# Kernel optimization log

Measured on AMD Instinct MI355X. Metric: run time of the kernel, lower is better.

The kernel has to match this reference:

```python
import jax, jax.numpy as jnp
import numpy as np

N = 50000      # nodes
D = 64         # hidden
EMB = 16       # emb_dims
E = 800000     # edges = N * knn(16)
R2 = 0.3 ** 2  # r^2 at epoch 0
GW = 1.0       # grav_weight at epoch 0
EPS = 1e-5


def _lin_params(k, fi, fo):
    kw, kb = jax.random.split(k)
    W = jax.random.normal(kw, (fi, fo), jnp.float32) / np.sqrt(fi).astype(np.float32)
    b = jax.random.normal(kb, (fo,), jnp.float32) * 0.01
    return W, b


def setup_inputs() -> dict:
    key = jax.random.key(0)
    ks = jax.random.split(key, 16)
    inp = {}
    inp['hidden_features'] = jax.random.normal(ks[0], (N, D), jnp.float32)
    inp['edge_index'] = jax.random.randint(ks[1], (2, E), 0, N, jnp.int32)
    inp['current_epoch'] = 0
    # spatial network: (D+1)->D->D->EMB, each Linear + LayerNorm + ReLU
    for i, (fi, fo) in enumerate([(D + 1, D), (D, D), (D, EMB)]):
        W, b = _lin_params(ks[2 + i], fi, fo)
        inp[f'sW{i}'] = W
        inp[f'sb{i}'] = b
        inp[f'sg{i}'] = jnp.ones((fo,), jnp.float32)
        inp[f'sB{i}'] = jnp.zeros((fo,), jnp.float32)
    # feature network: 2*(D+1)->D->D, each Linear + LayerNorm + ReLU
    for i, (fi, fo) in enumerate([(2 * (D + 1), D), (D, D)]):
        W, b = _lin_params(ks[8 + i], fi, fo)
        inp[f'fW{i}'] = W
        inp[f'fb{i}'] = b
        inp[f'fg{i}'] = jnp.ones((fo,), jnp.float32)
        inp[f'fB{i}'] = jnp.zeros((fo,), jnp.float32)
    return inp


def _ln(x, g, b):
    m = jnp.mean(x, axis=-1, keepdims=True)
    v = jnp.mean((x - m) ** 2, axis=-1, keepdims=True)
    return (x - m) * jax.lax.rsqrt(v + EPS) * g + b


def _blk(x, W, b, g, B):
    return jax.nn.relu(_ln(x @ W + b, g, B))


def reference(hidden_features, edge_index, current_epoch,
              sW0, sb0, sg0, sB0, sW1, sb1, sg1, sB1, sW2, sb2, sg2, sB2,
              fW0, fb0, fg0, fB0, fW1, fb1, fg1, fB1):
    # append per-node mean channel: [N, D] -> [N, D+1]
    h = jnp.concatenate([hidden_features,
                         jnp.mean(hidden_features, axis=1, keepdims=True)], axis=-1)
    # spatial embedding [N, EMB]
    s = _blk(_blk(_blk(h, sW0, sb0, sg0, sB0), sW1, sb1, sg1, sB1), sW2, sb2, sg2, sB2)
    start = edge_index[0]
    end = edge_index[1]
    # gravitational edge weight: exp(-grav_weight * ||s_i - s_j||^2 / r^2)
    d = jnp.sum((s[start] - s[end]) ** 2, axis=-1)  # [E]
    w = jnp.exp(-GW * d / R2)                        # [E]
    # gather -> weight -> scatter_add aggregation
    agg = jax.ops.segment_sum(h[start] * w[:, None], end, num_segments=h.shape[0])
    cat = jnp.concatenate([agg, h], axis=-1)  # [N, 2*(D+1)]
    out = _blk(_blk(cat, fW0, fb0, fg0, fB0), fW1, fb1, fg1, fB1)  # [N, D]
    return out, s
```

## Files before the change

kernel.cpp:

```cpp
#include <hip/hip_runtime.h>
#include <hip/hip_bf16.h>
#include <hip/hip_fp16.h>

#define NN 50000
#define DD 64
#define EMBD 16
#define EE 800000
#define TILES ((NN + 63) / 64)

#define BINW 64
#define NBIN 782
#define CHE 4096
#define NCH 196
#define CAPA 32
#define LCAP 64
#define PREPB 64

#define OW_S0 0
#define OW_S1 6656
#define OW_S2 11264
#define OW_F0 12416
#define OW_F1 23168
#define NWB   27776

typedef short s16x8 __attribute__((ext_vector_type(8)));
typedef float f32x4 __attribute__((ext_vector_type(4)));
typedef _Float16 h16x8 __attribute__((ext_vector_type(8)));

__device__ __forceinline__ unsigned short f2b(float x) {
  unsigned u = __float_as_uint(x);
  return (unsigned short)((u + 0x7FFFu + ((u >> 16) & 1u)) >> 16);
}

__device__ __forceinline__ float b2f(unsigned short u) {
  return __uint_as_float(((unsigned)u) << 16);
}

__device__ __forceinline__ unsigned short f2h(float x) {
  return __half_as_ushort(__float2half(x));
}

__device__ __forceinline__ float h2f(unsigned short u) {
  return (float)__ushort_as_half(u);
}

__device__ __forceinline__ float wred64f(float v) {
  v += __shfl_xor(v, 1);  v += __shfl_xor(v, 2);  v += __shfl_xor(v, 4);
  v += __shfl_xor(v, 8);  v += __shfl_xor(v, 16); v += __shfl_xor(v, 32);
  return v;
}

__global__ __launch_bounds__(512)
void GravConv3556_prebin_k(const int* __restrict__ ei,
                           const float* __restrict__ sW0, const float* __restrict__ sW1,
                           const float* __restrict__ sW2, const float* __restrict__ fW0,
                           const float* __restrict__ fW1,
                           unsigned short* __restrict__ wb,
                           unsigned* __restrict__ seg,
                           unsigned char* __restrict__ cnts)
{
  int tid = threadIdx.x;
  if ((int)blockIdx.x >= NCH) {
    int i0 = ((int)blockIdx.x - NCH) * 512 + tid;
    int st = PREPB * 512;
    for (int i = i0; i < 64 * 104; i += st) {
      int n = i / 104, k = i % 104;
      wb[OW_S0 + i] = (k < 65) ? f2b(sW0[k * 64 + n]) : (unsigned short)0;
    }
    for (int i = i0; i < 64 * 72; i += st) {
      int n = i / 72, k = i % 72;
      wb[OW_S1 + i] = (k < 64) ? f2b(sW1[k * 64 + n]) : (unsigned short)0;
    }
    for (int i = i0; i < 16 * 72; i += st) {
      int n = i / 72, k = i % 72;
      wb[OW_S2 + i] = (k < 64) ? f2b(sW2[k * 16 + n]) : (unsigned short)0;
    }
    for (int i = i0; i < 64 * 168; i += st) {
      int n = i / 168, k = i % 168;
      wb[OW_F0 + i] = (k < 130) ? f2b(fW0[k * 64 + n]) : (unsigned short)0;
    }
    for (int i = i0; i < 64 * 72; i += st) {
      int n = i / 72, k = i % 72;
      wb[OW_F1 + i] = (k < 64) ? f2b(fW1[k * 64 + n]) : (unsigned short)0;
    }
    return;
  }
  __shared__ int bc[NBIN];
  int chunk = blockIdx.x;
  for (int i = tid; i < NBIN; i += 512) bc[i] = 0;
  __syncthreads();
  int e0 = chunk * CHE;
  int e1 = e0 + CHE; if (e1 > EE) e1 = EE;
  unsigned* segc = seg + (size_t)chunk * NBIN * CAPA;
  for (int e = e0 + tid; e < e1; e += 512) {
    int a = ei[e];
    int b = ei[EE + e];
    int bin = b >> 6;
    int pos = atomicAdd(&bc[bin], 1);
    if (pos < CAPA) segc[bin * CAPA + pos] = ((unsigned)a << 6) | (unsigned)(b & 63);
  }
  __syncthreads();
  for (int i = tid; i < NBIN; i += 512) {
    int c = bc[i]; if (c > CAPA) c = CAPA;
    cnts[(size_t)i * NCH + chunk] = (unsigned char)c;
  }
}

#define XROW 104
__global__ __launch_bounds__(256)
void GravConv3556_spatial_k(const float* __restrict__ hidden,
    const unsigned short* __restrict__ wb,
    const float* __restrict__ sb0, const float* __restrict__ sg0, const float* __restrict__ sB0,
    const float* __restrict__ sb1, const float* __restrict__ sg1, const float* __restrict__ sB1,
    const float* __restrict__ sb2, const float* __restrict__ sg2, const float* __restrict__ sB2,
    float* __restrict__ s_out, unsigned short* __restrict__ s16,
    unsigned short* __restrict__ hid16)
{
  __shared__ unsigned short X[64 * XROW];
  __shared__ unsigned short W0[64 * XROW];
  __shared__ unsigned short W1[64 * 72];
  __shared__ unsigned short W2[16 * 72];
  int tid = threadIdx.x;
  int lane = tid & 63;
  int wv = tid >> 6;
  int c = lane & 15;
  int q = lane >> 4;
  int base = blockIdx.x * 64;

  {
    const uint4* g = (const uint4*)(wb + OW_S0); uint4* l = (uint4*)W0;
    for (int i = tid; i < 832; i += 256) l[i] = g[i];
    g = (const uint4*)(wb + OW_S1); l = (uint4*)W1;
    for (int i = tid; i < 576; i += 256) l[i] = g[i];
    g = (const uint4*)(wb + OW_S2); l = (uint4*)W2;
    for (int i = tid; i < 144; i += 256) l[i] = g[i];
  }
  for (int i = 0; i < 16; i++) {
    int m = wv * 16 + i;
    int node = base + m; if (node >= NN) node = NN - 1;
    float x = hidden[(size_t)node * 64 + lane];
    float mean = wred64f(x) * (1.0f / 64.0f);
    X[m * XROW + lane] = f2b(x);
    hid16[(size_t)node * 64 + lane] = f2h(x);
    if (lane == 0) X[m * XROW + 64] = f2b(mean);
    if (lane < 39) X[m * XROW + 65 + lane] = 0;
  }
  __syncthreads();

  int mrow = wv * 16 + c;
  float z[16];

  {
    s16x8 a[3];
    #pragma unroll
    for (int kc = 0; kc < 3; kc++)
      a[kc] = *(const s16x8*)(X + mrow * XROW + kc * 32 + q * 8);
    #pragma unroll
    for (int nt = 0; nt < 4; nt++) {
      f32x4 acc = {0.f, 0.f, 0.f, 0.f};
      #pragma unroll
      for (int kc = 0; kc < 3; kc++) {
        s16x8 b = *(const s16x8*)(W0 + (nt * 16 + c) * XROW + kc * 32 + q * 8);
        acc = __builtin_amdgcn_mfma_f32_16x16x32_bf16(a[kc], b, acc, 0, 0, 0);
      }
      float bias = sb0[nt * 16 + c];
      #pragma unroll
      for (int reg = 0; reg < 4; reg++) z[nt * 4 + reg] = acc[reg] + bias;
    }
    #pragma unroll
    for (int reg = 0; reg < 4; reg++) {
      float s1 = z[reg] + z[4 + reg] + z[8 + reg] + z[12 + reg];
      float s2 = z[reg] * z[reg] + z[4 + reg] * z[4 + reg]
               + z[8 + reg] * z[8 + reg] + z[12 + reg] * z[12 + reg];
      s1 += __shfl_xor(s1, 1); s2 += __shfl_xor(s2, 1);
      s1 += __shfl_xor(s1, 2); s2 += __shfl_xor(s2, 2);
      s1 += __shfl_xor(s1, 4); s2 += __shfl_xor(s2, 4);
      s1 += __shfl_xor(s1, 8); s2 += __shfl_xor(s2, 8);
      float mu = s1 * (1.0f / 64.0f);
      float rs = rsqrtf(fmaxf(s2 * (1.0f / 64.0f) - mu * mu, 0.f) + 1e-5f);
      int m = wv * 16 + q * 4 + reg;
      #pragma unroll
      for (int nt = 0; nt < 4; nt++) {
        int n = nt * 16 + c;
        float y = fmaxf(fmaf((z[nt * 4 + reg] - mu) * rs, sg0[n], sB0[n]), 0.f);
        X[m * XROW + n] = f2b(y);
      }
    }
  }

  {
    s16x8 a[2];
    #pragma unroll
    for (int kc = 0; kc < 2; kc++)
      a[kc] = *(const s16x8*)(X + mrow * XROW + kc * 32 + q * 8);
    #pragma unroll
    for (int nt = 0; nt < 4; nt++) {
      f32x4 acc = {0.f, 0.f, 0.f, 0.f};
      #pragma unroll
      for (int kc = 0; kc < 2; kc++) {
        s16x8 b = *(const s16x8*)(W1 + (nt * 16 + c) * 72 + kc * 32 + q * 8);
        acc = __builtin_amdgcn_mfma_f32_16x16x32_bf16(a[kc], b, acc, 0, 0, 0);
      }
      float bias = sb1[nt * 16 + c];
      #pragma unroll
      for (int reg = 0; reg < 4; reg++) z[nt * 4 + reg] = acc[reg] + bias;
    }
    #pragma unroll
    for (int reg = 0; reg < 4; reg++) {
      float s1 = z[reg] + z[4 + reg] + z[8 + reg] + z[12 + reg];
      float s2 = z[reg] * z[reg] + z[4 + reg] * z[4 + reg]
               + z[8 + reg] * z[8 + reg] + z[12 + reg] * z[12 + reg];
      s1 += __shfl_xor(s1, 1); s2 += __shfl_xor(s2, 1);
      s1 += __shfl_xor(s1, 2); s2 += __shfl_xor(s2, 2);
      s1 += __shfl_xor(s1, 4); s2 += __shfl_xor(s2, 4);
      s1 += __shfl_xor(s1, 8); s2 += __shfl_xor(s2, 8);
      float mu = s1 * (1.0f / 64.0f);
      float rs = rsqrtf(fmaxf(s2 * (1.0f / 64.0f) - mu * mu, 0.f) + 1e-5f);
      int m = wv * 16 + q * 4 + reg;
      #pragma unroll
      for (int nt = 0; nt < 4; nt++) {
        int n = nt * 16 + c;
        float y = fmaxf(fmaf((z[nt * 4 + reg] - mu) * rs, sg1[n], sB1[n]), 0.f);
        X[m * XROW + n] = f2b(y);
      }
    }
  }

  {
    s16x8 a[2];
    #pragma unroll
    for (int kc = 0; kc < 2; kc++)
      a[kc] = *(const s16x8*)(X + mrow * XROW + kc * 32 + q * 8);
    f32x4 acc = {0.f, 0.f, 0.f, 0.f};
    #pragma unroll
    for (int kc = 0; kc < 2; kc++) {
      s16x8 b = *(const s16x8*)(W2 + c * 72 + kc * 32 + q * 8);
      acc = __builtin_amdgcn_mfma_f32_16x16x32_bf16(a[kc], b, acc, 0, 0, 0);
    }
    float bias = sb2[c];
    float z4[4];
    #pragma unroll
    for (int reg = 0; reg < 4; reg++) z4[reg] = acc[reg] + bias;
    #pragma unroll
    for (int reg = 0; reg < 4; reg++) {
      float s1 = z4[reg], s2 = z4[reg] * z4[reg];
      s1 += __shfl_xor(s1, 1); s2 += __shfl_xor(s2, 1);
      s1 += __shfl_xor(s1, 2); s2 += __shfl_xor(s2, 2);
      s1 += __shfl_xor(s1, 4); s2 += __shfl_xor(s2, 4);
      s1 += __shfl_xor(s1, 8); s2 += __shfl_xor(s2, 8);
      float mu = s1 * (1.0f / 16.0f);
      float rs = rsqrtf(fmaxf(s2 * (1.0f / 16.0f) - mu * mu, 0.f) + 1e-5f);
      float y = fmaxf(fmaf((z4[reg] - mu) * rs, sg2[c], sB2[c]), 0.f);
      int node = base + wv * 16 + q * 4 + reg;
      if (node < NN) {
        s_out[(size_t)node * 16 + c] = y;
        s16[(size_t)node * 16 + c] = f2h(y);
      }
    }
  }
}

#define CROW 168
__global__ __launch_bounds__(1024)
void GravConv3556_featagg_k(const float* __restrict__ hidden,
    const unsigned short* __restrict__ hid16, const unsigned short* __restrict__ s16,
    const unsigned* __restrict__ seg, const unsigned char* __restrict__ cnts,
    const unsigned short* __restrict__ wb,
    const float* __restrict__ fb0, const float* __restrict__ fg0, const float* __restrict__ fB0,
    const float* __restrict__ fb1, const float* __restrict__ fg1, const float* __restrict__ fB1,
    float* __restrict__ out)
{
  __shared__ unsigned short catB[64 * CROW];
  __shared__ unsigned short W0T[64 * CROW];
  __shared__ unsigned short W1T[64 * 72];
  __shared__ unsigned short lbuk[64 * LCAP];
  __shared__ int lcnt[64];
  int tid = threadIdx.x;
  int lane = tid & 63;
  int wv = tid >> 6;
  int bin = blockIdx.x;
  int base = bin * 64;

  {
    const uint4* g = (const uint4*)(wb + OW_F0); uint4* l = (uint4*)W0T;
    for (int i = tid; i < 1344; i += 1024) l[i] = g[i];
    g = (const uint4*)(wb + OW_F1); l = (uint4*)W1T;
    for (int i = tid; i < 576; i += 1024) l[i] = g[i];
  }
  for (int i = tid; i < 64; i += 1024) lcnt[i] = 0;
  __syncthreads();

  const unsigned char* cr = cnts + (size_t)bin * NCH;
  for (int c = wv; c < NCH; c += 16) {
    int k = cr[c];
    if (lane < k) {
      unsigned e = seg[((size_t)c * NBIN + bin) * CAPA + lane];
      int dl = (int)(e & 63u);
      int pos = atomicAdd(&lcnt[dl], 1);
      if (pos < LCAP) lbuk[dl * LCAP + pos] = (unsigned short)(e >> 6);
    }
  }
  __syncthreads();

  const _Float16* hid = (const _Float16*)hid16;
  const _Float16* s = (const _Float16*)s16;
  for (int rn = wv; rn < 64; rn += 16) {
    int node = base + rn;
    int nclamp = node < NN ? node : NN - 1;
    int m = lcnt[rn]; if (m > LCAP) m = LCAP;
    unsigned pr = 0;
    if (lane < m) {
      int a = lbuk[rn * LCAP + lane];
      const h16x8* sa = (const h16x8*)(s + (size_t)a * 16);
      const h16x8* sn = (const h16x8*)(s + (size_t)node * 16);
      h16x8 p0 = sa[0], p1 = sa[1];
      h16x8 q0 = sn[0], q1 = sn[1];
      float d = 0.f;
      #pragma unroll
      for (int t = 0; t < 8; t++) {
        float u = (float)p0[t] - (float)q0[t];
        d = fmaf(u, u, d);
        float v = (float)p1[t] - (float)q1[t];
        d = fmaf(v, v, d);
      }
      float w = __expf(d * (-1.0f / 0.09f));
      pr = ((unsigned)a << 16) | (unsigned)f2h(w);
    }
    float xa0 = 0.f, xa1 = 0.f, xa2 = 0.f, xa3 = 0.f;
#define GSTEP(q, ACC) { int jj = jb + (q); int jc = jj < m ? jj : m - 1;        \
    unsigned u_ = (unsigned)__builtin_amdgcn_readlane((int)pr, jc);             \
    int   a_ = (int)(u_ >> 16);                                                 \
    float w_ = (jj < m) ? h2f((unsigned short)(u_ & 0xFFFFu)) : 0.0f;           \
    ACC = fmaf(w_, (float)hid[(size_t)a_ * 64 + lane], ACC); }
    for (int jb = 0; jb < m; jb += 8) {
      GSTEP(0, xa0) GSTEP(1, xa1) GSTEP(2, xa2) GSTEP(3, xa3)
      GSTEP(4, xa0) GSTEP(5, xa1) GSTEP(6, xa2) GSTEP(7, xa3)
    }
#undef GSTEP
    float xa = (xa0 + xa1) + (xa2 + xa3);
    float mA = wred64f(xa) * (1.0f / 64.0f);
    catB[rn * CROW + lane] = f2b(xa);
    float xh = hidden[(size_t)nclamp * 64 + lane];
    float mB = wred64f(xh) * (1.0f / 64.0f);
    catB[rn * CROW + 65 + lane] = f2b(xh);
    if (lane == 0) {
      catB[rn * CROW + 64] = f2b(mA);
      catB[rn * CROW + 129] = f2b(mB);
    }
    if (lane < 38) catB[rn * CROW + 130 + lane] = 0;
  }
  __syncthreads();

  if (wv < 4) {
    int c = lane & 15;
    int q = lane >> 4;
    int mrow = wv * 16 + c;

    s16x8 a0[5];
    #pragma unroll
    for (int kc = 0; kc < 5; kc++)
      a0[kc] = *(const s16x8*)(catB + mrow * CROW + kc * 32 + q * 8);

    float z[16];
    #pragma unroll
    for (int nt = 0; nt < 4; nt++) {
      f32x4 acc = {0.f, 0.f, 0.f, 0.f};
      #pragma unroll
      for (int kc = 0; kc < 5; kc++) {
        s16x8 b = *(const s16x8*)(W0T + (nt * 16 + c) * CROW + kc * 32 + q * 8);
        acc = __builtin_amdgcn_mfma_f32_16x16x32_bf16(a0[kc], b, acc, 0, 0, 0);
      }
      float bias = fb0[nt * 16 + c];
      #pragma unroll
      for (int reg = 0; reg < 4; reg++) z[nt * 4 + reg] = acc[reg] + bias;
    }
    #pragma unroll
    for (int reg = 0; reg < 4; reg++) {
      float s1 = z[reg] + z[4 + reg] + z[8 + reg] + z[12 + reg];
      float s2 = z[reg] * z[reg] + z[4 + reg] * z[4 + reg]
               + z[8 + reg] * z[8 + reg] + z[12 + reg] * z[12 + reg];
      s1 += __shfl_xor(s1, 1); s2 += __shfl_xor(s2, 1);
      s1 += __shfl_xor(s1, 2); s2 += __shfl_xor(s2, 2);
      s1 += __shfl_xor(s1, 4); s2 += __shfl_xor(s2, 4);
      s1 += __shfl_xor(s1, 8); s2 += __shfl_xor(s2, 8);
      float mu = s1 * (1.0f / 64.0f);
      float rs = rsqrtf(fmaxf(s2 * (1.0f / 64.0f) - mu * mu, 0.f) + 1e-5f);
      int m = wv * 16 + q * 4 + reg;
      #pragma unroll
      for (int nt = 0; nt < 4; nt++) {
        int n = nt * 16 + c;
        float y = fmaxf(fmaf((z[nt * 4 + reg] - mu) * rs, fg0[n], fB0[n]), 0.f);
        catB[m * CROW + n] = f2b(y);
      }
    }

    s16x8 a1[2];
    #pragma unroll
    for (int kc = 0; kc < 2; kc++)
      a1[kc] = *(const s16x8*)(catB + mrow * CROW + kc * 32 + q * 8);

    #pragma unroll
    for (int nt = 0; nt < 4; nt++) {
      f32x4 acc = {0.f, 0.f, 0.f, 0.f};
      #pragma unroll
      for (int kc = 0; kc < 2; kc++) {
        s16x8 b = *(const s16x8*)(W1T + (nt * 16 + c) * 72 + kc * 32 + q * 8);
        acc = __builtin_amdgcn_mfma_f32_16x16x32_bf16(a1[kc], b, acc, 0, 0, 0);
      }
      float bias = fb1[nt * 16 + c];
      #pragma unroll
      for (int reg = 0; reg < 4; reg++) z[nt * 4 + reg] = acc[reg] + bias;
    }
    #pragma unroll
    for (int reg = 0; reg < 4; reg++) {
      float s1 = z[reg] + z[4 + reg] + z[8 + reg] + z[12 + reg];
      float s2 = z[reg] * z[reg] + z[4 + reg] * z[4 + reg]
               + z[8 + reg] * z[8 + reg] + z[12 + reg] * z[12 + reg];
      s1 += __shfl_xor(s1, 1); s2 += __shfl_xor(s2, 1);
      s1 += __shfl_xor(s1, 2); s2 += __shfl_xor(s2, 2);
      s1 += __shfl_xor(s1, 4); s2 += __shfl_xor(s2, 4);
      s1 += __shfl_xor(s1, 8); s2 += __shfl_xor(s2, 8);
      float mu = s1 * (1.0f / 64.0f);
      float rs = rsqrtf(fmaxf(s2 * (1.0f / 64.0f) - mu * mu, 0.f) + 1e-5f);
      int node = base + wv * 16 + q * 4 + reg;
      if (node < NN) {
        #pragma unroll
        for (int nt = 0; nt < 4; nt++) {
          int n = nt * 16 + c;
          float y = fmaxf(fmaf((z[nt * 4 + reg] - mu) * rs, fg1[n], fB1[n]), 0.f);
          out[(size_t)node * 64 + n] = y;
        }
      }
    }
  }
}

extern "C" void kernel_launch(void* const* d_in, const int* in_sizes, int n_in,
                              void* d_out, int out_size, void* d_ws, size_t ws_size,
                              hipStream_t stream) {
  const float* hidden = (const float*)d_in[0];
  const int*   ei     = (const int*)d_in[1];
  const float *sW0 = (const float*)d_in[3],  *sb0 = (const float*)d_in[4],
              *sg0 = (const float*)d_in[5],  *sB0 = (const float*)d_in[6];
  const float *sW1 = (const float*)d_in[7],  *sb1 = (const float*)d_in[8],
              *sg1 = (const float*)d_in[9],  *sB1 = (const float*)d_in[10];
  const float *sW2 = (const float*)d_in[11], *sb2 = (const float*)d_in[12],
              *sg2 = (const float*)d_in[13], *sB2 = (const float*)d_in[14];
  const float *fW0 = (const float*)d_in[15], *fb0 = (const float*)d_in[16],
              *fg0 = (const float*)d_in[17], *fB0 = (const float*)d_in[18];
  const float *fW1 = (const float*)d_in[19], *fb1 = (const float*)d_in[20],
              *fg1 = (const float*)d_in[21], *fB1 = (const float*)d_in[22];

  float* out   = (float*)d_out;
  float* s_out = out + (size_t)NN * 64;

  unsigned* seg = (unsigned*)d_ws;
  unsigned char* cnts = (unsigned char*)(seg + (size_t)NCH * NBIN * CAPA);
  unsigned short* hid16 = (unsigned short*)
      (((uintptr_t)(cnts + (size_t)NBIN * NCH) + 15) & ~(uintptr_t)15);
  unsigned short* s16   = hid16 + (size_t)NN * 64;
  unsigned short* wbuf  = s16 + (size_t)NN * 16;

  GravConv3556_prebin_k<<<NCH + PREPB, 512, 0, stream>>>(ei, sW0, sW1, sW2, fW0, fW1,
                                                         wbuf, seg, cnts);
  GravConv3556_spatial_k<<<TILES, 256, 0, stream>>>(hidden, wbuf,
      sb0, sg0, sB0, sb1, sg1, sB1, sb2, sg2, sB2, s_out, s16, hid16);
  GravConv3556_featagg_k<<<NBIN, 1024, 0, stream>>>(hidden, hid16, s16, seg, cnts,
      wbuf, fb0, fg0, fB0, fb1, fg1, fB1, out);
}
```

Baseline: 199.3 us.

## Balance edge aggregation across waves with flat edge list and LDS atomics

Replaces per-destination-node edge buckets (one wave per node, padded to multiples of 8) with a flat per-bin edge list. Edge weights are computed by all threads in parallel, using a shared cache of the bin's node embeddings. Each wave then handles 64 edges and scatters into an LDS accumulator with float atomics, which removes load imbalance from skewed in-degrees. The cost is LDS atomic contention, extra syncs, and weights staged into LDS reused by aliasing. It also adds nondeterministic summation order and caps each bin at 1280 edges.

```diff
diff --git a/kernel.cpp b/kernel.cpp
--- a/kernel.cpp
+++ b/kernel.cpp
@@ -13,7 +13,7 @@
 #define CHE 4096
 #define NCH 196
 #define CAPA 32
-#define LCAP 64
+#define ECAP 1280
 #define PREPB 64
 
 #define OW_S0 0
@@ -271,83 +271,104 @@
     float* __restrict__ out)
 {
   __shared__ unsigned short catB[64 * CROW];
-  __shared__ unsigned short W0T[64 * CROW];
-  __shared__ unsigned short W1T[64 * 72];
-  __shared__ unsigned short lbuk[64 * LCAP];
-  __shared__ int lcnt[64];
+  __shared__ char sm1[30720] __attribute__((aligned(16)));
+  __shared__ int ecnt_s;
+  float* lacc           = (float*)sm1;
+  unsigned* eflat       = (unsigned*)(sm1 + 16384);
+  unsigned short* wflat = (unsigned short*)(sm1 + 21504);
+  unsigned short* scache= (unsigned short*)(sm1 + 24064);
+  unsigned short* W0T   = (unsigned short*)sm1;
+  unsigned short* W1T   = (unsigned short*)(sm1 + 21504);
+
   int tid = threadIdx.x;
   int lane = tid & 63;
   int wv = tid >> 6;
   int bin = blockIdx.x;
   int base = bin * 64;
 
+  if (tid == 0) ecnt_s = 0;
+  for (int i = tid; i < 4096; i += 1024) lacc[i] = 0.f;
+  if (tid < 512) {
+    int nodeIdx = tid >> 3;
+    int nclamp = base + nodeIdx; if (nclamp >= NN) nclamp = NN - 1;
+    ((unsigned*)scache)[tid] = ((const unsigned*)s16)[nclamp * 8 + (tid & 7)];
+  }
+  for (int rn = wv; rn < 64; rn += 16) {
+    int node = base + rn;
+    int nclamp = node < NN ? node : NN - 1;
+    float xh = hidden[(size_t)nclamp * 64 + lane];
+    float mB = wred64f(xh) * (1.0f / 64.0f);
+    catB[rn * CROW + 65 + lane] = f2b(xh);
+    if (lane == 0) catB[rn * CROW + 129] = f2b(mB);
+    if (lane < 38) catB[rn * CROW + 130 + lane] = 0;
+  }
+  __syncthreads();
+
+  const unsigned char* cr = cnts + (size_t)bin * NCH;
+  for (int c2 = wv; c2 < NCH; c2 += 16) {
+    int k = cr[c2];
+    if (lane < k) {
+      unsigned e = seg[((size_t)c2 * NBIN + bin) * CAPA + lane];
+      int pos = atomicAdd(&ecnt_s, 1);
+      if (pos < ECAP) eflat[pos] = e;
+    }
+  }
+  __syncthreads();
+  int ec = ecnt_s; if (ec > ECAP) ec = ECAP;
+
+  const _Float16* sg2p = (const _Float16*)s16;
+  for (int i = tid; i < ec; i += 1024) {
+    unsigned e = eflat[i];
+    int a = (int)(e >> 6);
+    int dl = (int)(e & 63u);
+    const h16x8* sa = (const h16x8*)(sg2p + (size_t)a * 16);
+    h16x8 p0 = sa[0], p1 = sa[1];
+    h16x8 q0 = *(const h16x8*)(scache + dl * 16);
+    h16x8 q1 = *(const h16x8*)(scache + dl * 16 + 8);
+    float d = 0.f;
+    #pragma unroll
+    for (int t = 0; t < 8; t++) {
+      float u = (float)p0[t] - (float)q0[t];
+      d = fmaf(u, u, d);
+      float v = (float)p1[t] - (float)q1[t];
+      d = fmaf(v, v, d);
+    }
+    wflat[i] = f2h(__expf(d * (-1.0f / 0.09f)));
+  }
+  __syncthreads();
+
+  const _Float16* hid = (const _Float16*)hid16;
+  for (int c0 = wv * 64; c0 < ec; c0 += 1024) {
+    int rem = ec - c0; if (rem > 64) rem = 64;
+    unsigned ev = 0; unsigned wvv = 0;
+    if (lane < rem) { ev = eflat[c0 + lane]; wvv = wflat[c0 + lane]; }
+#define SSTEP(j) { int jj = (j); if (jj < rem) {                                \
+      unsigned e_ = (unsigned)__builtin_amdgcn_readlane((int)ev, jj);           \
+      float w_ = h2f((unsigned short)__builtin_amdgcn_readlane((int)wvv, jj));  \
+      int a_ = (int)(e_ >> 6); int d_ = (int)(e_ & 63u);                        \
+      float hv = (float)hid[(size_t)a_ * 64 + lane];                            \
+      atomicAdd(&lacc[d_ * 64 + lane], w_ * hv); } }
+    for (int jb = 0; jb < rem; jb += 8) {
+      SSTEP(jb + 0) SSTEP(jb + 1) SSTEP(jb + 2) SSTEP(jb + 3)
+      SSTEP(jb + 4) SSTEP(jb + 5) SSTEP(jb + 6) SSTEP(jb + 7)
+    }
+#undef SSTEP
+  }
+  __syncthreads();
+
+  for (int rn = wv; rn < 64; rn += 16) {
+    float xa = lacc[rn * 64 + lane];
+    float mA = wred64f(xa) * (1.0f / 64.0f);
+    catB[rn * CROW + lane] = f2b(xa);
+    if (lane == 0) catB[rn * CROW + 64] = f2b(mA);
+  }
+  __syncthreads();
+
   {
     const uint4* g = (const uint4*)(wb + OW_F0); uint4* l = (uint4*)W0T;
     for (int i = tid; i < 1344; i += 1024) l[i] = g[i];
     g = (const uint4*)(wb + OW_F1); l = (uint4*)W1T;
     for (int i = tid; i < 576; i += 1024) l[i] = g[i];
-  }
-  for (int i = tid; i < 64; i += 1024) lcnt[i] = 0;
-  __syncthreads();
-
-  const unsigned char* cr = cnts + (size_t)bin * NCH;
-  for (int c = wv; c < NCH; c += 16) {
-    int k = cr[c];
-    if (lane < k) {
-      unsigned e = seg[((size_t)c * NBIN + bin) * CAPA + lane];
-      int dl = (int)(e & 63u);
-      int pos = atomicAdd(&lcnt[dl], 1);
-      if (pos < LCAP) lbuk[dl * LCAP + pos] = (unsigned short)(e >> 6);
-    }
-  }
-  __syncthreads();
-
-  const _Float16* hid = (const _Float16*)hid16;
-  const _Float16* s = (const _Float16*)s16;
-  for (int rn = wv; rn < 64; rn += 16) {
-    int node = base + rn;
-    int nclamp = node < NN ? node : NN - 1;
-    int m = lcnt[rn]; if (m > LCAP) m = LCAP;
-    unsigned pr = 0;
-    if (lane < m) {
-      int a = lbuk[rn * LCAP + lane];
-      const h16x8* sa = (const h16x8*)(s + (size_t)a * 16);
-      const h16x8* sn = (const h16x8*)(s + (size_t)node * 16);
-      h16x8 p0 = sa[0], p1 = sa[1];
-      h16x8 q0 = sn[0], q1 = sn[1];
-      float d = 0.f;
-      #pragma unroll
-      for (int t = 0; t < 8; t++) {
-        float u = (float)p0[t] - (float)q0[t];
-        d = fmaf(u, u, d);
-        float v = (float)p1[t] - (float)q1[t];
-        d = fmaf(v, v, d);
-      }
-      float w = __expf(d * (-1.0f / 0.09f));
-      pr = ((unsigned)a << 16) | (unsigned)f2h(w);
-    }
-    float xa0 = 0.f, xa1 = 0.f, xa2 = 0.f, xa3 = 0.f;
-#define GSTEP(q, ACC) { int jj = jb + (q); int jc = jj < m ? jj : m - 1;        \
-    unsigned u_ = (unsigned)__builtin_amdgcn_readlane((int)pr, jc);             \
-    int   a_ = (int)(u_ >> 16);                                                 \
-    float w_ = (jj < m) ? h2f((unsigned short)(u_ & 0xFFFFu)) : 0.0f;           \
-    ACC = fmaf(w_, (float)hid[(size_t)a_ * 64 + lane], ACC); }
-    for (int jb = 0; jb < m; jb += 8) {
-      GSTEP(0, xa0) GSTEP(1, xa1) GSTEP(2, xa2) GSTEP(3, xa3)
-      GSTEP(4, xa0) GSTEP(5, xa1) GSTEP(6, xa2) GSTEP(7, xa3)
-    }
-#undef GSTEP
-    float xa = (xa0 + xa1) + (xa2 + xa3);
-    float mA = wred64f(xa) * (1.0f / 64.0f);
-    catB[rn * CROW + lane] = f2b(xa);
-    float xh = hidden[(size_t)nclamp * 64 + lane];
-    float mB = wred64f(xh) * (1.0f / 64.0f);
-    catB[rn * CROW + 65 + lane] = f2b(xh);
-    if (lane == 0) {
-      catB[rn * CROW + 64] = f2b(mA);
-      catB[rn * CROW + 129] = f2b(mB);
-    }
-    if (lane < 38) catB[rn * CROW + 130 + lane] = 0;
   }
   __syncthreads();
 
```

Result: slower. 534.4 us (+168.1%).

## Split fp16 hidden copy into two 32-channel planes for cache-friendlier gathers

Applied to the files above, without the earlier changes.

The fp16 copy of hidden features is stored as two planes of 32 channels each instead of 64-wide rows. The aggregation loop now gathers two neighbours per wave instruction (half-wave each) from one plane, then repeats the pass for the second plane. This is meant to shrink each plane's working set so gathers hit cache more often. The edge-segment and hidden-row reads also become nontemporal loads. In exchange it costs a second gather pass, extra readlanes and cross-half shuffles, and more live registers.

```diff
diff --git a/kernel.cpp b/kernel.cpp
--- a/kernel.cpp
+++ b/kernel.cpp
@@ -114,7 +114,7 @@
     const float* __restrict__ sb1, const float* __restrict__ sg1, const float* __restrict__ sB1,
     const float* __restrict__ sb2, const float* __restrict__ sg2, const float* __restrict__ sB2,
     float* __restrict__ s_out, unsigned short* __restrict__ s16,
-    unsigned short* __restrict__ hid16)
+    unsigned short* __restrict__ hplanes)
 {
   __shared__ unsigned short X[64 * XROW];
   __shared__ unsigned short W0[64 * XROW];
@@ -141,7 +141,7 @@
     float x = hidden[(size_t)node * 64 + lane];
     float mean = wred64f(x) * (1.0f / 64.0f);
     X[m * XROW + lane] = f2b(x);
-    hid16[(size_t)node * 64 + lane] = f2h(x);
+    hplanes[(size_t)(lane >> 5) * (NN * 32) + (size_t)node * 32 + (lane & 31)] = f2h(x);
     if (lane == 0) X[m * XROW + 64] = f2b(mean);
     if (lane < 39) X[m * XROW + 65 + lane] = 0;
   }
@@ -263,7 +263,7 @@
 #define CROW 168
 __global__ __launch_bounds__(1024)
 void GravConv3556_featagg_k(const float* __restrict__ hidden,
-    const unsigned short* __restrict__ hid16, const unsigned short* __restrict__ s16,
+    const unsigned short* __restrict__ hplanes, const unsigned short* __restrict__ s16,
     const unsigned* __restrict__ seg, const unsigned char* __restrict__ cnts,
     const unsigned short* __restrict__ wb,
     const float* __restrict__ fb0, const float* __restrict__ fg0, const float* __restrict__ fB0,
@@ -291,10 +291,11 @@
   __syncthreads();
 
   const unsigned char* cr = cnts + (size_t)bin * NCH;
-  for (int c = wv; c < NCH; c += 16) {
-    int k = cr[c];
+  for (int c2 = wv; c2 < NCH; c2 += 16) {
+    int k = cr[c2];
     if (lane < k) {
-      unsigned e = seg[((size_t)c * NBIN + bin) * CAPA + lane];
+      unsigned e = __builtin_nontemporal_load(
+          &seg[((size_t)c2 * NBIN + bin) * CAPA + lane]);
       int dl = (int)(e & 63u);
       int pos = atomicAdd(&lcnt[dl], 1);
       if (pos < LCAP) lbuk[dl * LCAP + pos] = (unsigned short)(e >> 6);
@@ -302,9 +303,28 @@
   }
   __syncthreads();
 
-  const _Float16* hid = (const _Float16*)hid16;
+  const _Float16* pl0 = (const _Float16*)hplanes;
+  const _Float16* pl1 = pl0 + (size_t)NN * 32;
   const _Float16* s = (const _Float16*)s16;
-  for (int rn = wv; rn < 64; rn += 16) {
+  unsigned prx[4];
+  int mx[4];
+  float s1x[4];
+
+#define GPAIR(j0, ACC, PL) {                                                    \
+    int jA = jb + (j0); int jB = jA + 1;                                        \
+    int jcA = jA < m ? jA : m - 1; int jcB = jB < m ? jB : m - 1;               \
+    unsigned uA = (unsigned)__builtin_amdgcn_readlane((int)pr, jcA);            \
+    unsigned uB = (unsigned)__builtin_amdgcn_readlane((int)pr, jcB);            \
+    bool lo = lane < 32;                                                        \
+    unsigned u_ = lo ? uA : uB;                                                 \
+    int jj = lo ? jA : jB;                                                      \
+    float w_ = (jj < m) ? h2f((unsigned short)(u_ & 0xFFFFu)) : 0.0f;           \
+    float hv = (float)PL[(size_t)(u_ >> 16) * 32 + (lane & 31)];                \
+    ACC = fmaf(w_, hv, ACC); }
+
+  #pragma unroll
+  for (int i = 0; i < 4; i++) {
+    int rn = wv + 16 * i;
     int node = base + rn;
     int nclamp = node < NN ? node : NN - 1;
     int m = lcnt[rn]; if (m > LCAP) m = LCAP;
@@ -312,7 +332,7 @@
     if (lane < m) {
       int a = lbuk[rn * LCAP + lane];
       const h16x8* sa = (const h16x8*)(s + (size_t)a * 16);
-      const h16x8* sn = (const h16x8*)(s + (size_t)node * 16);
+      const h16x8* sn = (const h16x8*)(s + (size_t)nclamp * 16);
       h16x8 p0 = sa[0], p1 = sa[1];
       h16x8 q0 = sn[0], q1 = sn[1];
       float d = 0.f;
@@ -326,29 +346,40 @@
       float w = __expf(d * (-1.0f / 0.09f));
       pr = ((unsigned)a << 16) | (unsigned)f2h(w);
     }
-    float xa0 = 0.f, xa1 = 0.f, xa2 = 0.f, xa3 = 0.f;
-#define GSTEP(q, ACC) { int jj = jb + (q); int jc = jj < m ? jj : m - 1;        \
-    unsigned u_ = (unsigned)__builtin_amdgcn_readlane((int)pr, jc);             \
-    int   a_ = (int)(u_ >> 16);                                                 \
-    float w_ = (jj < m) ? h2f((unsigned short)(u_ & 0xFFFFu)) : 0.0f;           \
-    ACC = fmaf(w_, (float)hid[(size_t)a_ * 64 + lane], ACC); }
+    mx[i] = m; prx[i] = pr;
+    float xaA = 0.f, xaB = 0.f;
     for (int jb = 0; jb < m; jb += 8) {
-      GSTEP(0, xa0) GSTEP(1, xa1) GSTEP(2, xa2) GSTEP(3, xa3)
-      GSTEP(4, xa0) GSTEP(5, xa1) GSTEP(6, xa2) GSTEP(7, xa3)
-    }
-#undef GSTEP
-    float xa = (xa0 + xa1) + (xa2 + xa3);
-    float mA = wred64f(xa) * (1.0f / 64.0f);
-    catB[rn * CROW + lane] = f2b(xa);
-    float xh = hidden[(size_t)nclamp * 64 + lane];
+      GPAIR(0, xaA, pl0) GPAIR(2, xaB, pl0)
+      GPAIR(4, xaA, pl0) GPAIR(6, xaB, pl0)
+    }
+    float xa = xaA + xaB;
+    s1x[i] = wred64f(xa);
+    float tot = xa + __shfl_xor(xa, 32);
+    if (lane < 32) catB[rn * CROW + lane] = f2b(tot);
+    float xh = __builtin_nontemporal_load(&hidden[(size_t)nclamp * 64 + lane]);
     float mB = wred64f(xh) * (1.0f / 64.0f);
     catB[rn * CROW + 65 + lane] = f2b(xh);
-    if (lane == 0) {
-      catB[rn * CROW + 64] = f2b(mA);
-      catB[rn * CROW + 129] = f2b(mB);
-    }
+    if (lane == 0) catB[rn * CROW + 129] = f2b(mB);
     if (lane < 38) catB[rn * CROW + 130 + lane] = 0;
   }
+
+  #pragma unroll
+  for (int i = 0; i < 4; i++) {
+    int rn = wv + 16 * i;
+    int m = mx[i];
+    unsigned pr = prx[i];
+    float xaA = 0.f, xaB = 0.f;
+    for (int jb = 0; jb < m; jb += 8) {
+      GPAIR(0, xaA, pl1) GPAIR(2, xaB, pl1)
+      GPAIR(4, xaA, pl1) GPAIR(6, xaB, pl1)
+    }
+    float xa = xaA + xaB;
+    float tot = xa + __shfl_xor(xa, 32);
+    if (lane < 32) catB[rn * CROW + 32 + lane] = f2b(tot);
+    float stot = s1x[i] + wred64f(xa);
+    if (lane == 0) catB[rn * CROW + 64] = f2b(stot * (1.0f / 64.0f));
+  }
+#undef GPAIR
   __syncthreads();
 
   if (wv < 4) {
@@ -456,15 +487,15 @@
 
   unsigned* seg = (unsigned*)d_ws;
   unsigned char* cnts = (unsigned char*)(seg + (size_t)NCH * NBIN * CAPA);
-  unsigned short* hid16 = (unsigned short*)
+  unsigned short* hplanes = (unsigned short*)
       (((uintptr_t)(cnts + (size_t)NBIN * NCH) + 15) & ~(uintptr_t)15);
-  unsigned short* s16   = hid16 + (size_t)NN * 64;
+  unsigned short* s16   = hplanes + (size_t)NN * 64;
   unsigned short* wbuf  = s16 + (size_t)NN * 16;
 
   GravConv3556_prebin_k<<<NCH + PREPB, 512, 0, stream>>>(ei, sW0, sW1, sW2, fW0, fW1,
                                                          wbuf, seg, cnts);
   GravConv3556_spatial_k<<<TILES, 256, 0, stream>>>(hidden, wbuf,
-      sb0, sg0, sB0, sb1, sg1, sB1, sb2, sg2, sB2, s_out, s16, hid16);
-  GravConv3556_featagg_k<<<NBIN, 1024, 0, stream>>>(hidden, hid16, s16, seg, cnts,
+      sb0, sg0, sB0, sb1, sg1, sB1, sb2, sg2, sB2, s_out, s16, hplanes);
+  GravConv3556_featagg_k<<<NBIN, 1024, 0, stream>>>(hidden, hplanes, s16, seg, cnts,
       wbuf, fb0, fg0, fB0, fb1, fg1, fB1, out);
 }
```

Result: slower. 232.5 us (+16.6%).

## Merge edge binning and spatial MLP into one launch with per-block weight conversion

Applied to the files above, without the earlier changes.

Combines the edge prebinning kernel and the spatial-embedding kernel into a single launch whose block ranges do binning, feature-weight conversion, or spatial tiles, so the independent work overlaps and one launch plus one dependency boundary go away. Spatial blocks now convert their spatial weights from fp32 into shared memory directly instead of reading a pre-converted buffer, which adds redundant strided conversion work per tile. The binning blocks shrink from 512 to 256 threads. It also clamps the node index used for the destination embedding read in the aggregation kernel.

```diff
diff --git a/kernel.cpp b/kernel.cpp
--- a/kernel.cpp
+++ b/kernel.cpp
@@ -14,14 +14,11 @@
 #define NCH 196
 #define CAPA 32
 #define LCAP 64
-#define PREPB 64
-
-#define OW_S0 0
-#define OW_S1 6656
-#define OW_S2 11264
-#define OW_F0 12416
-#define OW_F1 23168
-#define NWB   27776
+#define FWB 8
+
+#define OW_F0 0
+#define OW_F1 10752
+#define NWB   15360
 
 typedef short s16x8 __attribute__((ext_vector_type(8)));
 typedef float f32x4 __attribute__((ext_vector_type(4)));
@@ -50,31 +47,50 @@
   return v;
 }
 
-__global__ __launch_bounds__(512)
-void GravConv3556_prebin_k(const int* __restrict__ ei,
-                           const float* __restrict__ sW0, const float* __restrict__ sW1,
-                           const float* __restrict__ sW2, const float* __restrict__ fW0,
-                           const float* __restrict__ fW1,
-                           unsigned short* __restrict__ wb,
-                           unsigned* __restrict__ seg,
-                           unsigned char* __restrict__ cnts)
+#define XROW 104
+__global__ __launch_bounds__(256)
+void GravConv3556_binspatial_k(const int* __restrict__ ei,
+    const float* __restrict__ hidden,
+    const float* __restrict__ sW0, const float* __restrict__ sW1,
+    const float* __restrict__ sW2, const float* __restrict__ fW0,
+    const float* __restrict__ fW1,
+    const float* __restrict__ sb0, const float* __restrict__ sg0, const float* __restrict__ sB0,
+    const float* __restrict__ sb1, const float* __restrict__ sg1, const float* __restrict__ sB1,
+    const float* __restrict__ sb2, const float* __restrict__ sg2, const float* __restrict__ sB2,
+    unsigned short* __restrict__ wb, unsigned* __restrict__ seg,
+    unsigned char* __restrict__ cnts,
+    float* __restrict__ s_out, unsigned short* __restrict__ s16,
+    unsigned short* __restrict__ hid16)
 {
+  __shared__ char smem[38144] __attribute__((aligned(16)));
   int tid = threadIdx.x;
-  if ((int)blockIdx.x >= NCH) {
-    int i0 = ((int)blockIdx.x - NCH) * 512 + tid;
-    int st = PREPB * 512;
-    for (int i = i0; i < 64 * 104; i += st) {
-      int n = i / 104, k = i % 104;
-      wb[OW_S0 + i] = (k < 65) ? f2b(sW0[k * 64 + n]) : (unsigned short)0;
-    }
-    for (int i = i0; i < 64 * 72; i += st) {
-      int n = i / 72, k = i % 72;
-      wb[OW_S1 + i] = (k < 64) ? f2b(sW1[k * 64 + n]) : (unsigned short)0;
-    }
-    for (int i = i0; i < 16 * 72; i += st) {
-      int n = i / 72, k = i % 72;
-      wb[OW_S2 + i] = (k < 64) ? f2b(sW2[k * 16 + n]) : (unsigned short)0;
-    }
+  int bid = blockIdx.x;
+
+  if (bid < NCH) {
+    int* bc = (int*)smem;
+    for (int i = tid; i < NBIN; i += 256) bc[i] = 0;
+    __syncthreads();
+    int e0 = bid * CHE;
+    int e1 = e0 + CHE; if (e1 > EE) e1 = EE;
+    unsigned* segc = seg + (size_t)bid * NBIN * CAPA;
+    for (int e = e0 + tid; e < e1; e += 256) {
+      int a = ei[e];
+      int b = ei[EE + e];
+      int bin = b >> 6;
+      int pos = atomicAdd(&bc[bin], 1);
+      if (pos < CAPA) segc[bin * CAPA + pos] = ((unsigned)a << 6) | (unsigned)(b & 63);
+    }
+    __syncthreads();
+    for (int i = tid; i < NBIN; i += 256) {
+      int c = bc[i]; if (c > CAPA) c = CAPA;
+      cnts[(size_t)i * NCH + bid] = (unsigned char)c;
+    }
+    return;
+  }
+
+  if (bid < NCH + FWB) {
+    int i0 = (bid - NCH) * 256 + tid;
+    int st = FWB * 256;
     for (int i = i0; i < 64 * 168; i += st) {
       int n = i / 168, k = i % 168;
       wb[OW_F0 + i] = (k < 130) ? f2b(fW0[k * 64 + n]) : (unsigned short)0;
@@ -85,55 +101,28 @@
     }
     return;
   }
-  __shared__ int bc[NBIN];
-  int chunk = blockIdx.x;
-  for (int i = tid; i < NBIN; i += 512) bc[i] = 0;
-  __syncthreads();
-  int e0 = chunk * CHE;
-  int e1 = e0 + CHE; if (e1 > EE) e1 = EE;
-  unsigned* segc = seg + (size_t)chunk * NBIN * CAPA;
-  for (int e = e0 + tid; e < e1; e += 512) {
-    int a = ei[e];
-    int b = ei[EE + e];
-    int bin = b >> 6;
-    int pos = atomicAdd(&bc[bin], 1);
-    if (pos < CAPA) segc[bin * CAPA + pos] = ((unsigned)a << 6) | (unsigned)(b & 63);
-  }
-  __syncthreads();
-  for (int i = tid; i < NBIN; i += 512) {
-    int c = bc[i]; if (c > CAPA) c = CAPA;
-    cnts[(size_t)i * NCH + chunk] = (unsigned char)c;
-  }
-}
-
-#define XROW 104
-__global__ __launch_bounds__(256)
-void GravConv3556_spatial_k(const float* __restrict__ hidden,
-    const unsigned short* __restrict__ wb,
-    const float* __restrict__ sb0, const float* __restrict__ sg0, const float* __restrict__ sB0,
-    const float* __restrict__ sb1, const float* __restrict__ sg1, const float* __restrict__ sB1,
-    const float* __restrict__ sb2, const float* __restrict__ sg2, const float* __restrict__ sB2,
-    float* __restrict__ s_out, unsigned short* __restrict__ s16,
-    unsigned short* __restrict__ hid16)
-{
-  __shared__ unsigned short X[64 * XROW];
-  __shared__ unsigned short W0[64 * XROW];
-  __shared__ unsigned short W1[64 * 72];
-  __shared__ unsigned short W2[16 * 72];
-  int tid = threadIdx.x;
+
+  unsigned short* X  = (unsigned short*)smem;
+  unsigned short* W0 = X + 64 * XROW;
+  unsigned short* W1 = W0 + 64 * XROW;
+  unsigned short* W2 = W1 + 64 * 72;
   int lane = tid & 63;
   int wv = tid >> 6;
   int c = lane & 15;
   int q = lane >> 4;
-  int base = blockIdx.x * 64;
-
-  {
-    const uint4* g = (const uint4*)(wb + OW_S0); uint4* l = (uint4*)W0;
-    for (int i = tid; i < 832; i += 256) l[i] = g[i];
-    g = (const uint4*)(wb + OW_S1); l = (uint4*)W1;
-    for (int i = tid; i < 576; i += 256) l[i] = g[i];
-    g = (const uint4*)(wb + OW_S2); l = (uint4*)W2;
-    for (int i = tid; i < 144; i += 256) l[i] = g[i];
+  int base = (bid - NCH - FWB) * 64;
+
+  for (int i = tid; i < 64 * 104; i += 256) {
+    int n = i / 104, k = i % 104;
+    W0[i] = (k < 65) ? f2b(sW0[k * 64 + n]) : (unsigned short)0;
+  }
+  for (int i = tid; i < 64 * 72; i += 256) {
+    int n = i / 72, k = i % 72;
+    W1[i] = (k < 64) ? f2b(sW1[k * 64 + n]) : (unsigned short)0;
+  }
+  for (int i = tid; i < 16 * 72; i += 256) {
+    int n = i / 72, k = i % 72;
+    W2[i] = (k < 64) ? f2b(sW2[k * 16 + n]) : (unsigned short)0;
   }
   for (int i = 0; i < 16; i++) {
     int m = wv * 16 + i;
@@ -291,10 +280,10 @@
   __syncthreads();
 
   const unsigned char* cr = cnts + (size_t)bin * NCH;
-  for (int c = wv; c < NCH; c += 16) {
-    int k = cr[c];
+  for (int c2 = wv; c2 < NCH; c2 += 16) {
+    int k = cr[c2];
     if (lane < k) {
-      unsigned e = seg[((size_t)c * NBIN + bin) * CAPA + lane];
+      unsigned e = seg[((size_t)c2 * NBIN + bin) * CAPA + lane];
       int dl = (int)(e & 63u);
       int pos = atomicAdd(&lcnt[dl], 1);
       if (pos < LCAP) lbuk[dl * LCAP + pos] = (unsigned short)(e >> 6);
@@ -312,7 +301,7 @@
     if (lane < m) {
       int a = lbuk[rn * LCAP + lane];
       const h16x8* sa = (const h16x8*)(s + (size_t)a * 16);
-      const h16x8* sn = (const h16x8*)(s + (size_t)node * 16);
+      const h16x8* sn = (const h16x8*)(s + (size_t)nclamp * 16);
       h16x8 p0 = sa[0], p1 = sa[1];
       h16x8 q0 = sn[0], q1 = sn[1];
       float d = 0.f;
@@ -461,10 +450,10 @@
   unsigned short* s16   = hid16 + (size_t)NN * 64;
   unsigned short* wbuf  = s16 + (size_t)NN * 16;
 
-  GravConv3556_prebin_k<<<NCH + PREPB, 512, 0, stream>>>(ei, sW0, sW1, sW2, fW0, fW1,
-                                                         wbuf, seg, cnts);
-  GravConv3556_spatial_k<<<TILES, 256, 0, stream>>>(hidden, wbuf,
-      sb0, sg0, sB0, sb1, sg1, sB1, sb2, sg2, sB2, s_out, s16, hid16);
+  GravConv3556_binspatial_k<<<NCH + FWB + TILES, 256, 0, stream>>>(ei, hidden,
+      sW0, sW1, sW2, fW0, fW1,
+      sb0, sg0, sB0, sb1, sg1, sB1, sb2, sg2, sB2,
+      wbuf, seg, cnts, s_out, s16, hid16);
   GravConv3556_featagg_k<<<NBIN, 1024, 0, stream>>>(hidden, hid16, s16, seg, cnts,
       wbuf, fb0, fg0, fB0, fb1, fg1, fB1, out);
 }
```

Result: slower. 206.9 us (+3.8%).
